# Optimization experiments

Measured on AMD Instinct MI355X. Metric: run time of the kernel, lower is better.

## Reference

```python
import jax, jax.numpy as jnp
import numpy as np

B, T, C = 2, 2048, 1024
N = 16
D = C // N  # 64


def setup_inputs() -> dict:
    key = jax.random.key(0)
    ks = jax.random.split(key, 5)
    s = 1.0 / np.sqrt(C)  # lecun_normal-ish scale for Dense kernels
    return {
        "src": jax.random.normal(ks[0], (B, T, C), jnp.float32),
        "mask": jnp.ones((B, T), jnp.float32),  # unused on causal path
        "Wq": jax.random.normal(ks[1], (C, C), jnp.float32) * s,
        "bq": jnp.zeros((C,), jnp.float32),
        "Wk": jax.random.normal(ks[2], (C, C), jnp.float32) * s,
        "bk": jnp.zeros((C,), jnp.float32),
        "Wv": jax.random.normal(ks[3], (C, C), jnp.float32) * s,
        "bv": jnp.zeros((C,), jnp.float32),
        "Wo": jax.random.normal(ks[4], (C, C), jnp.float32) * s,
        "bo": jnp.zeros((C,), jnp.float32),
    }


def reference(src, mask, Wq, bq, Wk, bk, Wv, bv, Wo, bo):
    # QKV projections -> [B, N, T, D]
    def heads(x):
        return x.reshape(B, T, N, D).transpose(0, 2, 1, 3)

    q = heads(src @ Wq + bq)
    k = heads(src @ Wk + bk)
    v = heads(src @ Wv + bv)

    # scores [B, N, T, T], causal mask, softmax
    scores = jnp.einsum("bntd,bnsd->bnts", q, k) / jnp.sqrt(jnp.float32(D))
    causal = jnp.tril(jnp.ones((T, T), bool))
    scores = jnp.where(causal, scores, -jnp.inf)
    attn = jax.nn.softmax(scores, axis=-1)

    # weighted values, merge heads, output projection (dropout deterministic)
    out = jnp.einsum("bnts,bnsd->bntd", attn, v)
    out = out.transpose(0, 2, 1, 3).reshape(B, T, C)
    return out @ Wo + bo
```

## Files before the change

### kernel.cpp

```cpp
#include <hip/hip_runtime.h>

typedef __bf16 bf16;
typedef bf16 bf16x8 __attribute__((ext_vector_type(8)));
typedef float f32x4 __attribute__((ext_vector_type(4)));
typedef unsigned short u16;
typedef u16 u16x4 __attribute__((ext_vector_type(4)));

typedef const __attribute__((address_space(1))) void* gptr_t;
typedef __attribute__((address_space(3))) void* sptr_t;

__device__ __forceinline__ void async16(const void* g, void* l) {
  __builtin_amdgcn_global_load_lds((gptr_t)g, (sptr_t)l, 16, 0, 0);
}
__device__ __forceinline__ u16 f2bf(float v) {
  return __builtin_bit_cast(u16, (bf16)v);
}

__global__ void kTransW(const float* __restrict__ Wq, const float* __restrict__ Wk,
                        const float* __restrict__ Wv, const float* __restrict__ Wo,
                        u16* __restrict__ Wt) {
  __shared__ float tile[32][33];
  const int z = blockIdx.z;
  const float* src = (z == 0) ? Wq : (z == 1) ? Wk : (z == 2) ? Wv : Wo;
  const int n0 = blockIdx.x * 32, k0 = blockIdx.y * 32;
  const int tx = threadIdx.x, ty = threadIdx.y;
#pragma unroll
  for (int j = 0; j < 4; ++j)
    tile[ty + j * 8][tx] = src[(size_t)(k0 + ty + j * 8) * 1024 + n0 + tx];
  __syncthreads();
#pragma unroll
  for (int j = 0; j < 4; ++j)
    Wt[(size_t)z * 1048576 + (size_t)(n0 + ty + j * 8) * 1024 + k0 + tx] =
        f2bf(tile[tx][ty + j * 8]);
}

__global__ void kPack(const float* __restrict__ x, u16* __restrict__ y) {
  const int i = (blockIdx.x * 256 + threadIdx.x) * 4;
  float4 v = *(const float4*)&x[i];
  u16x4 o = {f2bf(v.x), f2bf(v.y), f2bf(v.z), f2bf(v.w)};
  *(u16x4*)&y[i] = o;
}

template <int EPI>
__global__ __launch_bounds__(256, 2) void kGemm(
    const u16* __restrict__ A, const u16* __restrict__ Bt,
    const float* __restrict__ b0, const float* __restrict__ b1,
    const float* __restrict__ b2, u16* __restrict__ outQ,
    float* __restrict__ outF) {
  __shared__ __align__(16) u16 As[128 * 32];
  __shared__ __align__(16) u16 Bs[128 * 32];
  const int tid = threadIdx.x, l = tid & 63, w = tid >> 6;
  const int mb = blockIdx.x & 31, nb = blockIdx.x >> 5;
  const int mbase = mb * 128, nbase = nb * 128;
  const int wr = (w >> 1) * 64, wc = (w & 1) * 64;
  f32x4 acc[4][4];
#pragma unroll
  for (int i = 0; i < 4; ++i)
#pragma unroll
    for (int j = 0; j < 4; ++j) acc[i][j] = (f32x4){0.f, 0.f, 0.f, 0.f};

  for (int kt = 0; kt < 32; ++kt) {
    __syncthreads();
#pragma unroll
    for (int i = 0; i < 2; ++i) {
      const int q = (w * 2 + i) * 64 + l;
      const int r = q >> 2, sl = q & 3;
      const int ksw = (sl ^ ((r >> 1) & 3)) * 8;
      async16(&A[(size_t)(mbase + r) * 1024 + kt * 32 + ksw], &As[(w * 2 + i) * 512]);
      async16(&Bt[(size_t)(nbase + r) * 1024 + kt * 32 + ksw], &Bs[(w * 2 + i) * 512]);
    }
    __syncthreads();
    bf16x8 a[4], b[4];
#pragma unroll
    for (int mf = 0; mf < 4; ++mf) {
      const int row = wr + mf * 16 + (l & 15);
      const int slot = (l >> 4) ^ ((row >> 1) & 3);
      a[mf] = *(const bf16x8*)&As[row * 32 + slot * 8];
    }
#pragma unroll
    for (int nf = 0; nf < 4; ++nf) {
      const int row = wc + nf * 16 + (l & 15);
      const int slot = (l >> 4) ^ ((row >> 1) & 3);
      b[nf] = *(const bf16x8*)&Bs[row * 32 + slot * 8];
    }
#pragma unroll
    for (int mf = 0; mf < 4; ++mf)
#pragma unroll
      for (int nf = 0; nf < 4; ++nf)
        acc[mf][nf] = __builtin_amdgcn_mfma_f32_16x16x32_bf16(a[mf], b[nf],
                                                              acc[mf][nf], 0, 0, 0);
  }

  if constexpr (EPI == 0) {
    const int mat = nb >> 3;
    const float* bias = (mat == 0) ? b0 : (mat == 1) ? b1 : b2;
    const float qscale = (mat == 0) ? 0.1803368801f : 1.0f;
    u16* Qo = outQ;
    u16* Ko = outQ + 4 * 1048576;
    u16* Vo = outQ + 8 * 1048576;
#pragma unroll
    for (int nf = 0; nf < 4; ++nf) {
      const int n = nbase + wc + nf * 16 + (l & 15);
      const int c = n & 1023, h = c >> 6, d = c & 63;
      const float bsv = bias[c];
#pragma unroll
      for (int mf = 0; mf < 4; ++mf)
#pragma unroll
        for (int r = 0; r < 4; ++r) {
          const int m = mbase + wr + mf * 16 + (l >> 4) * 4 + r;
          const int bb = m >> 11, t = m & 2047;
          const u16 hv = f2bf((acc[mf][nf][r] + bsv) * qscale);
          if (mat == 0)
            Qo[((size_t)(bb * 16 + h) * 2048 + t) * 64 + d] = hv;
          else if (mat == 1)
            Ko[((size_t)(bb * 16 + h) * 2048 + t) * 64 + d] = hv;
          else
            Vo[((size_t)(bb * 16 + h) * 64 + d) * 2048 + t] = hv;
        }
    }
  } else {
#pragma unroll
    for (int nf = 0; nf < 4; ++nf) {
      const int n = nbase + wc + nf * 16 + (l & 15);
      const float bsv = b0[n];
#pragma unroll
      for (int mf = 0; mf < 4; ++mf)
#pragma unroll
        for (int r = 0; r < 4; ++r) {
          const int m = mbase + wr + mf * 16 + (l >> 4) * 4 + r;
          outF[(size_t)m * 1024 + n] = acc[mf][nf][r] + bsv;
        }
    }
  }
}

#define PSTR 88
__global__ __launch_bounds__(256, 2) void kAttn(const u16* __restrict__ Q,
                                                const u16* __restrict__ K,
                                                const u16* __restrict__ Vt,
                                                u16* __restrict__ AO) {
  __shared__ __align__(16) u16 Ksh[2][64 * 64];
  __shared__ __align__(16) u16 Vsh[2][64 * 64];
  __shared__ __align__(16) u16 Pl[4][16 * PSTR];
  const int tid = threadIdx.x, l = tid & 63, w = tid >> 6;
  const int g = l >> 4, c = l & 15;
  const int pi = blockIdx.x, bh = blockIdx.y;
  const int qtA = pi, qtB = 31 - pi;
  const size_t head = (size_t)bh * 131072;

  bf16x8 aqA[2], aqB[2];
  {
    const int qrA = qtA * 64 + w * 16 + c;
    const int qrB = qtB * 64 + w * 16 + c;
#pragma unroll
    for (int ks = 0; ks < 2; ++ks) {
      aqA[ks] = *(const bf16x8*)&Q[head + (size_t)qrA * 64 + ks * 32 + g * 8];
      aqB[ks] = *(const bf16x8*)&Q[head + (size_t)qrB * 64 + ks * 32 + g * 8];
    }
  }

  f32x4 accA[4], accB[4];
#pragma unroll
  for (int i = 0; i < 4; ++i) {
    accA[i] = (f32x4){0.f, 0.f, 0.f, 0.f};
    accB[i] = (f32x4){0.f, 0.f, 0.f, 0.f};
  }
  float mA = -__builtin_inff(), lA_ = 0.f;
  float mB = -__builtin_inff(), lB_ = 0.f;

  auto stage = [&](int bufi, int st) {
#pragma unroll
    for (int i = 0; i < 2; ++i) {
      const int q = (w * 2 + i) * 64 + l;
      const int r = q >> 3, sl = q & 7;
      const int ksw = (sl ^ (r & 7)) * 8;
      async16(&K[head + (size_t)(st * 64 + r) * 64 + ksw], &Ksh[bufi][(w * 2 + i) * 512]);
      async16(&Vt[head + (size_t)r * 2048 + st * 64 + ksw], &Vsh[bufi][(w * 2 + i) * 512]);
    }
  };

  auto computeTile = [&](int st, int qt, bf16x8* aq, f32x4* accO, float& mcol,
                         float& lcol, int cur) {
    f32x4 sT[4];
#pragma unroll
    for (int i = 0; i < 4; ++i) sT[i] = (f32x4){0.f, 0.f, 0.f, 0.f};
#pragma unroll
    for (int ks = 0; ks < 2; ++ks)
#pragma unroll
      for (int nf = 0; nf < 4; ++nf) {
        const int row = nf * 16 + c;
        const int slot = (ks * 4 + g) ^ (row & 7);
        bf16x8 bk = *(const bf16x8*)&Ksh[cur][row * 64 + slot * 8];
        sT[nf] = __builtin_amdgcn_mfma_f32_16x16x32_bf16(bk, aq[ks], sT[nf], 0, 0, 0);
      }

    float v[16];
#pragma unroll
    for (int nf = 0; nf < 4; ++nf)
#pragma unroll
      for (int r = 0; r < 4; ++r) v[nf * 4 + r] = sT[nf][r];
    if (st == qt) {
      const int qg = w * 16 + c;
#pragma unroll
      for (int nf = 0; nf < 4; ++nf)
#pragma unroll
        for (int r = 0; r < 4; ++r)
          if (nf * 16 + g * 4 + r > qg) v[nf * 4 + r] = -__builtin_inff();
    }

    float t0 = fmaxf(v[0], v[1]), t1 = fmaxf(v[2], v[3]);
    float t2 = fmaxf(v[4], v[5]), t3 = fmaxf(v[6], v[7]);
    float t4 = fmaxf(v[8], v[9]), t5 = fmaxf(v[10], v[11]);
    float t6 = fmaxf(v[12], v[13]), t7 = fmaxf(v[14], v[15]);
    float tm = fmaxf(fmaxf(fmaxf(t0, t1), fmaxf(t2, t3)),
                     fmaxf(fmaxf(t4, t5), fmaxf(t6, t7)));
    tm = fmaxf(tm, __shfl_xor(tm, 16));
    tm = fmaxf(tm, __shfl_xor(tm, 32));
    const float mnew = fmaxf(mcol, tm);
    const float corr = __builtin_exp2f(mcol - mnew);

    float p[16];
#pragma unroll
    for (int i = 0; i < 16; ++i) p[i] = __builtin_exp2f(v[i] - mnew);
#pragma unroll
    for (int nf = 0; nf < 4; ++nf) {
      u16x4 q4 = {f2bf(p[nf * 4 + 0]), f2bf(p[nf * 4 + 1]),
                  f2bf(p[nf * 4 + 2]), f2bf(p[nf * 4 + 3])};
      *(u16x4*)&Pl[w][c * PSTR + nf * 16 + g * 4] = q4;
    }
    float s0 = (p[0] + p[1]) + (p[2] + p[3]);
    float s1 = (p[4] + p[5]) + (p[6] + p[7]);
    float s2 = (p[8] + p[9]) + (p[10] + p[11]);
    float s3 = (p[12] + p[13]) + (p[14] + p[15]);
    float ps = (s0 + s1) + (s2 + s3);
    ps += __shfl_xor(ps, 16);
    ps += __shfl_xor(ps, 32);
    lcol = lcol * corr + ps;
    mcol = mnew;

#pragma unroll
    for (int r = 0; r < 4; ++r) {
      const float cr = __shfl(corr, g * 4 + r);
#pragma unroll
      for (int nd = 0; nd < 4; ++nd) accO[nd][r] *= cr;
    }

#pragma unroll
    for (int ks2 = 0; ks2 < 2; ++ks2) {
      bf16x8 pf = *(const bf16x8*)&Pl[w][c * PSTR + ks2 * 32 + g * 8];
#pragma unroll
      for (int nd = 0; nd < 4; ++nd) {
        const int row = nd * 16 + c;
        const int slot = (ks2 * 4 + g) ^ (row & 7);
        bf16x8 vf = *(const bf16x8*)&Vsh[cur][row * 64 + slot * 8];
        accO[nd] = __builtin_amdgcn_mfma_f32_16x16x32_bf16(pf, vf, accO[nd], 0, 0, 0);
      }
    }
  };

  stage(0, 0);
  for (int st = 0; st <= qtB; ++st) {
    const int cur = st & 1;
    if (st < qtB) {
      stage(cur ^ 1, st + 1);
      asm volatile("s_waitcnt vmcnt(4)" ::: "memory");
    } else {
      asm volatile("s_waitcnt vmcnt(0)" ::: "memory");
    }
    __builtin_amdgcn_s_barrier();
    __builtin_amdgcn_sched_barrier(0);

    computeTile(st, qtB, aqB, accB, mB, lB_, cur);
    if (st <= qtA) computeTile(st, qtA, aqA, accA, mA, lA_, cur);

    __builtin_amdgcn_s_barrier();
  }

  const int b = bh >> 4, h = bh & 15;
  auto writeOut = [&](int qt, f32x4* accO, float lcol) {
#pragma unroll
    for (int r = 0; r < 4; ++r) {
      const float lr = __shfl(lcol, g * 4 + r);
      const float rin = 1.0f / lr;
      const int t = qt * 64 + w * 16 + g * 4 + r;
#pragma unroll
      for (int nd = 0; nd < 4; ++nd)
        AO[(size_t)(b * 2048 + t) * 1024 + h * 64 + nd * 16 + c] =
            f2bf(accO[nd][r] * rin);
    }
  };
  writeOut(qtA, accA, lA_);
  writeOut(qtB, accB, lB_);
}

extern "C" void kernel_launch(void* const* d_in, const int* in_sizes, int n_in,
                              void* d_out, int out_size, void* d_ws, size_t ws_size,
                              hipStream_t stream) {
  const float* src = (const float*)d_in[0];
  const float* Wq = (const float*)d_in[2];
  const float* bq = (const float*)d_in[3];
  const float* Wk = (const float*)d_in[4];
  const float* bk = (const float*)d_in[5];
  const float* Wv = (const float*)d_in[6];
  const float* bv = (const float*)d_in[7];
  const float* Wo = (const float*)d_in[8];
  const float* bo = (const float*)d_in[9];
  float* out = (float*)d_out;

  char* ws = (char*)d_ws;
  u16* Wt = (u16*)(ws);
  u16* Xs = (u16*)(ws + 8ull * 1024 * 1024);
  u16* Qb = (u16*)(ws + 16ull * 1024 * 1024);
  u16* AO = (u16*)(ws + 40ull * 1024 * 1024);

  kTransW<<<dim3(32, 32, 4), dim3(32, 8), 0, stream>>>(Wq, Wk, Wv, Wo, Wt);
  kPack<<<dim3(4096), dim3(256), 0, stream>>>(src, Xs);
  kGemm<0><<<dim3(32 * 24), dim3(256), 0, stream>>>(Xs, Wt, bq, bk, bv, Qb, nullptr);
  kAttn<<<dim3(16, 32), dim3(256), 0, stream>>>(Qb, Qb + 4 * 1048576,
                                                Qb + 8 * 1048576, AO);
  kGemm<1><<<dim3(32 * 8), dim3(256), 0, stream>>>(AO, Wt + 3ull * 1048576, bo,
                                                   nullptr, nullptr, nullptr, out);
}
```

Measured before the change: 127.2 us.

## Double-buffer GEMM LDS tiles and interleave paired attention tiles

Result: slower. 130.3 us (+2.4%).

```diff
diff --git a/kernel.cpp b/kernel.cpp
--- a/kernel.cpp
+++ b/kernel.cpp
@@ -47,8 +47,8 @@
     const float* __restrict__ b0, const float* __restrict__ b1,
     const float* __restrict__ b2, u16* __restrict__ outQ,
     float* __restrict__ outF) {
-  __shared__ __align__(16) u16 As[128 * 32];
-  __shared__ __align__(16) u16 Bs[128 * 32];
+  __shared__ __align__(16) u16 As[2][128 * 32];
+  __shared__ __align__(16) u16 Bs[2][128 * 32];
   const int tid = threadIdx.x, l = tid & 63, w = tid >> 6;
   const int mb = blockIdx.x & 31, nb = blockIdx.x >> 5;
   const int mbase = mb * 128, nbase = nb * 128;
@@ -59,29 +59,43 @@
 #pragma unroll
     for (int j = 0; j < 4; ++j) acc[i][j] = (f32x4){0.f, 0.f, 0.f, 0.f};
 
-  for (int kt = 0; kt < 32; ++kt) {
-    __syncthreads();
+  auto stage = [&](int bufi, int kt) {
 #pragma unroll
     for (int i = 0; i < 2; ++i) {
       const int q = (w * 2 + i) * 64 + l;
       const int r = q >> 2, sl = q & 3;
       const int ksw = (sl ^ ((r >> 1) & 3)) * 8;
-      async16(&A[(size_t)(mbase + r) * 1024 + kt * 32 + ksw], &As[(w * 2 + i) * 512]);
-      async16(&Bt[(size_t)(nbase + r) * 1024 + kt * 32 + ksw], &Bs[(w * 2 + i) * 512]);
-    }
-    __syncthreads();
+      async16(&A[(size_t)(mbase + r) * 1024 + kt * 32 + ksw],
+              &As[bufi][(w * 2 + i) * 512]);
+      async16(&Bt[(size_t)(nbase + r) * 1024 + kt * 32 + ksw],
+              &Bs[bufi][(w * 2 + i) * 512]);
+    }
+  };
+
+  stage(0, 0);
+  for (int kt = 0; kt < 32; ++kt) {
+    const int cur = kt & 1;
+    if (kt < 31) {
+      stage(cur ^ 1, kt + 1);
+      asm volatile("s_waitcnt vmcnt(4)" ::: "memory");
+    } else {
+      asm volatile("s_waitcnt vmcnt(0)" ::: "memory");
+    }
+    __builtin_amdgcn_s_barrier();
+    __builtin_amdgcn_sched_barrier(0);
+
     bf16x8 a[4], b[4];
 #pragma unroll
     for (int mf = 0; mf < 4; ++mf) {
       const int row = wr + mf * 16 + (l & 15);
       const int slot = (l >> 4) ^ ((row >> 1) & 3);
-      a[mf] = *(const bf16x8*)&As[row * 32 + slot * 8];
+      a[mf] = *(const bf16x8*)&As[cur][row * 32 + slot * 8];
     }
 #pragma unroll
     for (int nf = 0; nf < 4; ++nf) {
       const int row = wc + nf * 16 + (l & 15);
       const int slot = (l >> 4) ^ ((row >> 1) & 3);
-      b[nf] = *(const bf16x8*)&Bs[row * 32 + slot * 8];
+      b[nf] = *(const bf16x8*)&Bs[cur][row * 32 + slot * 8];
     }
 #pragma unroll
     for (int mf = 0; mf < 4; ++mf)
@@ -89,6 +103,7 @@
       for (int nf = 0; nf < 4; ++nf)
         acc[mf][nf] = __builtin_amdgcn_mfma_f32_16x16x32_bf16(a[mf], b[nf],
                                                               acc[mf][nf], 0, 0, 0);
+    __builtin_amdgcn_s_barrier();
   }
 
   if constexpr (EPI == 0) {
@@ -134,14 +149,14 @@
   }
 }
 
-#define PSTR 88
+#define PSTR 72
 __global__ __launch_bounds__(256, 2) void kAttn(const u16* __restrict__ Q,
                                                 const u16* __restrict__ K,
                                                 const u16* __restrict__ Vt,
                                                 u16* __restrict__ AO) {
   __shared__ __align__(16) u16 Ksh[2][64 * 64];
   __shared__ __align__(16) u16 Vsh[2][64 * 64];
-  __shared__ __align__(16) u16 Pl[4][16 * PSTR];
+  __shared__ __align__(16) u16 Pl[4][2][16 * PSTR];
   const int tid = threadIdx.x, l = tid & 63, w = tid >> 6;
   const int g = l >> 4, c = l & 15;
   const int pi = blockIdx.x, bh = blockIdx.y;
@@ -179,35 +194,7 @@
     }
   };
 
-  auto computeTile = [&](int st, int qt, bf16x8* aq, f32x4* accO, float& mcol,
-                         float& lcol, int cur) {
-    f32x4 sT[4];
-#pragma unroll
-    for (int i = 0; i < 4; ++i) sT[i] = (f32x4){0.f, 0.f, 0.f, 0.f};
-#pragma unroll
-    for (int ks = 0; ks < 2; ++ks)
-#pragma unroll
-      for (int nf = 0; nf < 4; ++nf) {
-        const int row = nf * 16 + c;
-        const int slot = (ks * 4 + g) ^ (row & 7);
-        bf16x8 bk = *(const bf16x8*)&Ksh[cur][row * 64 + slot * 8];
-        sT[nf] = __builtin_amdgcn_mfma_f32_16x16x32_bf16(bk, aq[ks], sT[nf], 0, 0, 0);
-      }
-
-    float v[16];
-#pragma unroll
-    for (int nf = 0; nf < 4; ++nf)
-#pragma unroll
-      for (int r = 0; r < 4; ++r) v[nf * 4 + r] = sT[nf][r];
-    if (st == qt) {
-      const int qg = w * 16 + c;
-#pragma unroll
-      for (int nf = 0; nf < 4; ++nf)
-#pragma unroll
-        for (int r = 0; r < 4; ++r)
-          if (nf * 16 + g * 4 + r > qg) v[nf * 4 + r] = -__builtin_inff();
-    }
-
+  auto softmax16 = [&](float* v, float& mcol, float& lcol, float& corr, u16* Pw) {
     float t0 = fmaxf(v[0], v[1]), t1 = fmaxf(v[2], v[3]);
     float t2 = fmaxf(v[4], v[5]), t3 = fmaxf(v[6], v[7]);
     float t4 = fmaxf(v[8], v[9]), t5 = fmaxf(v[10], v[11]);
@@ -217,8 +204,7 @@
     tm = fmaxf(tm, __shfl_xor(tm, 16));
     tm = fmaxf(tm, __shfl_xor(tm, 32));
     const float mnew = fmaxf(mcol, tm);
-    const float corr = __builtin_exp2f(mcol - mnew);
-
+    corr = __builtin_exp2f(mcol - mnew);
     float p[16];
 #pragma unroll
     for (int i = 0; i < 16; ++i) p[i] = __builtin_exp2f(v[i] - mnew);
@@ -226,7 +212,7 @@
     for (int nf = 0; nf < 4; ++nf) {
       u16x4 q4 = {f2bf(p[nf * 4 + 0]), f2bf(p[nf * 4 + 1]),
                   f2bf(p[nf * 4 + 2]), f2bf(p[nf * 4 + 3])};
-      *(u16x4*)&Pl[w][c * PSTR + nf * 16 + g * 4] = q4;
+      *(u16x4*)&Pw[c * PSTR + ((nf ^ (c & 3)) * 16) + g * 4] = q4;
     }
     float s0 = (p[0] + p[1]) + (p[2] + p[3]);
     float s1 = (p[4] + p[5]) + (p[6] + p[7]);
@@ -237,17 +223,54 @@
     ps += __shfl_xor(ps, 32);
     lcol = lcol * corr + ps;
     mcol = mnew;
-
+  };
+
+  auto pread = [&](const u16* Pw, int ks2) -> bf16x8 {
+    const int so = ((8 * ks2 + 2 * g) ^ ((c & 3) << 2)) * 4;
+    return *(const bf16x8*)&Pw[c * PSTR + so];
+  };
+
+  auto computeOne = [&](int st, int qt, bf16x8* aq, f32x4* accO, float& mcol,
+                        float& lcol, int cur) {
+    f32x4 sT[4];
+#pragma unroll
+    for (int i = 0; i < 4; ++i) sT[i] = (f32x4){0.f, 0.f, 0.f, 0.f};
+    __builtin_amdgcn_s_setprio(1);
+#pragma unroll
+    for (int ks = 0; ks < 2; ++ks)
+#pragma unroll
+      for (int nf = 0; nf < 4; ++nf) {
+        const int row = nf * 16 + c;
+        const int slot = (ks * 4 + g) ^ (row & 7);
+        bf16x8 bk = *(const bf16x8*)&Ksh[cur][row * 64 + slot * 8];
+        sT[nf] = __builtin_amdgcn_mfma_f32_16x16x32_bf16(bk, aq[ks], sT[nf], 0, 0, 0);
+      }
+    __builtin_amdgcn_s_setprio(0);
+    float v[16];
+#pragma unroll
+    for (int nf = 0; nf < 4; ++nf)
+#pragma unroll
+      for (int r = 0; r < 4; ++r) v[nf * 4 + r] = sT[nf][r];
+    if (st == qt) {
+      const int qg = w * 16 + c;
+#pragma unroll
+      for (int nf = 0; nf < 4; ++nf)
+#pragma unroll
+        for (int r = 0; r < 4; ++r)
+          if (nf * 16 + g * 4 + r > qg) v[nf * 4 + r] = -__builtin_inff();
+    }
+    float corr;
+    softmax16(v, mcol, lcol, corr, &Pl[w][0][0]);
 #pragma unroll
     for (int r = 0; r < 4; ++r) {
       const float cr = __shfl(corr, g * 4 + r);
 #pragma unroll
       for (int nd = 0; nd < 4; ++nd) accO[nd][r] *= cr;
     }
-
+    __builtin_amdgcn_s_setprio(1);
 #pragma unroll
     for (int ks2 = 0; ks2 < 2; ++ks2) {
-      bf16x8 pf = *(const bf16x8*)&Pl[w][c * PSTR + ks2 * 32 + g * 8];
+      bf16x8 pf = pread(&Pl[w][0][0], ks2);
 #pragma unroll
       for (int nd = 0; nd < 4; ++nd) {
         const int row = nd * 16 + c;
@@ -256,6 +279,72 @@
         accO[nd] = __builtin_amdgcn_mfma_f32_16x16x32_bf16(pf, vf, accO[nd], 0, 0, 0);
       }
     }
+    __builtin_amdgcn_s_setprio(0);
+  };
+
+  auto computePair = [&](int st, int cur) {
+    f32x4 sB[4], sA[4];
+#pragma unroll
+    for (int i = 0; i < 4; ++i) {
+      sB[i] = (f32x4){0.f, 0.f, 0.f, 0.f};
+      sA[i] = (f32x4){0.f, 0.f, 0.f, 0.f};
+    }
+    __builtin_amdgcn_s_setprio(1);
+#pragma unroll
+    for (int ks = 0; ks < 2; ++ks)
+#pragma unroll
+      for (int nf = 0; nf < 4; ++nf) {
+        const int row = nf * 16 + c;
+        const int slot = (ks * 4 + g) ^ (row & 7);
+        bf16x8 bk = *(const bf16x8*)&Ksh[cur][row * 64 + slot * 8];
+        sB[nf] = __builtin_amdgcn_mfma_f32_16x16x32_bf16(bk, aqB[ks], sB[nf], 0, 0, 0);
+        sA[nf] = __builtin_amdgcn_mfma_f32_16x16x32_bf16(bk, aqA[ks], sA[nf], 0, 0, 0);
+      }
+    __builtin_amdgcn_s_setprio(0);
+    float vB[16], vA[16];
+#pragma unroll
+    for (int nf = 0; nf < 4; ++nf)
+#pragma unroll
+      for (int r = 0; r < 4; ++r) {
+        vB[nf * 4 + r] = sB[nf][r];
+        vA[nf * 4 + r] = sA[nf][r];
+      }
+    if (st == qtA) {
+      const int qg = w * 16 + c;
+#pragma unroll
+      for (int nf = 0; nf < 4; ++nf)
+#pragma unroll
+        for (int r = 0; r < 4; ++r)
+          if (nf * 16 + g * 4 + r > qg) vA[nf * 4 + r] = -__builtin_inff();
+    }
+    float corrB, corrA;
+    softmax16(vB, mB, lB_, corrB, &Pl[w][0][0]);
+    softmax16(vA, mA, lA_, corrA, &Pl[w][1][0]);
+#pragma unroll
+    for (int r = 0; r < 4; ++r) {
+      const float crB = __shfl(corrB, g * 4 + r);
+      const float crA = __shfl(corrA, g * 4 + r);
+#pragma unroll
+      for (int nd = 0; nd < 4; ++nd) {
+        accB[nd][r] *= crB;
+        accA[nd][r] *= crA;
+      }
+    }
+    __builtin_amdgcn_s_setprio(1);
+#pragma unroll
+    for (int ks2 = 0; ks2 < 2; ++ks2) {
+      bf16x8 pfB = pread(&Pl[w][0][0], ks2);
+      bf16x8 pfA = pread(&Pl[w][1][0], ks2);
+#pragma unroll
+      for (int nd = 0; nd < 4; ++nd) {
+        const int row = nd * 16 + c;
+        const int slot = (ks2 * 4 + g) ^ (row & 7);
+        bf16x8 vf = *(const bf16x8*)&Vsh[cur][row * 64 + slot * 8];
+        accB[nd] = __builtin_amdgcn_mfma_f32_16x16x32_bf16(pfB, vf, accB[nd], 0, 0, 0);
+        accA[nd] = __builtin_amdgcn_mfma_f32_16x16x32_bf16(pfA, vf, accA[nd], 0, 0, 0);
+      }
+    }
+    __builtin_amdgcn_s_setprio(0);
   };
 
   stage(0, 0);
@@ -270,8 +359,8 @@
     __builtin_amdgcn_s_barrier();
     __builtin_amdgcn_sched_barrier(0);
 
-    computeTile(st, qtB, aqB, accB, mB, lB_, cur);
-    if (st <= qtA) computeTile(st, qtA, aqA, accA, mA, lA_, cur);
+    if (st <= qtA) computePair(st, cur);
+    else computeOne(st, qtB, aqB, accB, mB, lB_, cur);
 
     __builtin_amdgcn_s_barrier();
   }
```
